# Kernel optimization log

Hardware: AMD Instinct MI355X
Metric: run time of the kernel (lower is better)

## Reference

```python
import jax, jax.numpy as jnp
import numpy as np

N, M, NTYPES, C, AXIS = 4096, 128, 2, 64, 16
TYPE_IDX = (0, 2048, 4096)        # atom-type partition along center axis
NTYPE_IDX = (0, 64, 128)          # neighbor-type partition along neighbor axis
RCUT = 6.0
BOX = 20.0
SR_MEAN = (0.1, 0.1)              # precomputed stats (get_stats)
SR_STD = (0.05, 0.05)
NORM = 20.0                       # avg neighbor count + 1


def setup_inputs() -> dict:
    key = jax.random.key(0)
    ks = jax.random.split(key, 16)
    coord_3N = jax.random.uniform(ks[0], (3, N), dtype=jnp.float32) * BOX
    box = jnp.full((3,), BOX, dtype=jnp.float32)
    # neighbors sorted by type: first 64 of type 0, last 64 of type 1
    nbr0 = jax.random.randint(ks[1], (N, M // 2), 0, TYPE_IDX[1])
    nbr1 = jax.random.randint(ks[2], (N, M // 2), TYPE_IDX[1], TYPE_IDX[2])
    nbrs_idx = jnp.concatenate([nbr0, nbr1], axis=1).astype(jnp.int32)
    # 4 per-(center,neighbor)-type embedding nets, widths 1->16->32->64, stacked
    eW0 = jax.random.normal(ks[3], (4, 1, 16), dtype=jnp.float32)
    eb0 = jax.random.normal(ks[4], (4, 16), dtype=jnp.float32) * 0.1
    eW1 = jax.random.normal(ks[5], (4, 16, 32), dtype=jnp.float32) / 4.0
    eb1 = jax.random.normal(ks[6], (4, 32), dtype=jnp.float32) * 0.1
    eW2 = jax.random.normal(ks[7], (4, 32, 64), dtype=jnp.float32) / (32.0 ** 0.5)
    eb2 = jax.random.normal(ks[8], (4, 64), dtype=jnp.float32) * 0.1
    Tbias = jnp.zeros((1, C), dtype=jnp.float32)
    # 2 per-type fitting nets, widths 1024->128->128->1, stacked
    fW0 = jax.random.normal(ks[9], (2, AXIS * C, 128), dtype=jnp.float32) / (AXIS * C) ** 0.5
    fb0 = jnp.zeros((2, 128), dtype=jnp.float32)
    fW1 = jax.random.normal(ks[10], (2, 128, 128), dtype=jnp.float32) / (128.0 ** 0.5)
    fb1 = jnp.zeros((2, 128), dtype=jnp.float32)
    fW2 = jax.random.normal(ks[11], (2, 128, 1), dtype=jnp.float32) / (128.0 ** 0.5)
    fb2 = jnp.zeros((2, 1), dtype=jnp.float32)
    Ebias = jnp.zeros((2,), dtype=jnp.float32)
    return {"coord_3N": coord_3N, "box": box, "nbrs_idx": nbrs_idx,
            "eW0": eW0, "eb0": eb0, "eW1": eW1, "eb1": eb1, "eW2": eW2, "eb2": eb2,
            "Tbias": Tbias, "fW0": fW0, "fb0": fb0, "fW1": fW1, "fb1": fb1,
            "fW2": fW2, "fb2": fb2, "Ebias": Ebias}


def reference(coord_3N, box, nbrs_idx, eW0, eb0, eW1, eb1, eW2, eb2,
              Tbias, fW0, fb0, fW1, fb1, fW2, fb2, Ebias):
    # --- neighbor gather + minimal-image relative coords (get_relative_coord) ---
    x_3NM = coord_3N[:, nbrs_idx] - coord_3N[:, :, None]            # [3,N,M]
    x_3NM = x_3NM - box[:, None, None] * jnp.round(x_3NM / box[:, None, None])
    r2 = (x_3NM ** 2).sum(0)
    mask = r2 > 1e-12
    rsafe = jnp.sqrt(jnp.where(mask, r2, 1.0))                      # safe for grads
    r_NM = jnp.where(mask, rsafe, 0.0)                              # [N,M]
    # --- smooth radial feature sr(r) = switch(r)/r ---
    sw = 0.5 * jnp.cos(jnp.pi * jnp.minimum(r_NM, RCUT) / RCUT) + 0.5
    sr_NM = jnp.where(mask & (r_NM < RCUT), sw / rsafe, 0.0)
    # --- per-center-type normalization (slice_t / concat_t over type_idx) ---
    srn_rows, srcn = [], []
    for i in range(NTYPES):
        blk = sr_NM[TYPE_IDX[i]:TYPE_IDX[i + 1]]
        srn_rows.append(blk / SR_STD[i])
        srcn.append((blk - SR_MEAN[i]) / SR_STD[i])
    sr_norm_NM = jnp.concatenate(srn_rows, 0)
    x_norm_3NM = x_3NM / jnp.where(mask, rsafe, 1.0)[None]
    R_3NM = 3 ** 0.5 * sr_norm_NM * x_norm_3NM
    R2diag_3NM = 9 ** 0.5 * sr_norm_NM * (x_norm_3NM ** 2 - 1.0 / 3.0)
    R2offd_3NM = 18 ** 0.5 * sr_norm_NM * (x_norm_3NM * jnp.stack([x_norm_3NM[1], x_norm_3NM[2], x_norm_3NM[0]]))
    R_XNM = jnp.concatenate([sr_norm_NM[None], R_3NM, R2diag_3NM, R2offd_3NM])  # [10,N,M]

    # --- per-(center,neighbor)-type embedding MLPs on scalar sr feature ---
    def embed(x, k):  # x: [n, m] -> [n, m, C]
        h = jnp.tanh(x[:, :, None] @ eW0[k] + eb0[k])
        h = jnp.tanh(h @ eW1[k] + eb1[k])
        return jnp.tanh(h @ eW2[k] + eb2[k])

    rows = []
    for i in range(NTYPES):
        cols = [embed(srcn[i][:, NTYPE_IDX[j]:NTYPE_IDX[j + 1]], i * NTYPES + j)
                for j in range(NTYPES)]
        rows.append(jnp.concatenate(cols, 1))
    embed_NMC = jnp.concatenate(rows, 0)                            # [N,M,C]

    # --- descriptor contraction ---
    T_NXC = jnp.einsum('xnm,nmc->nxc', R_XNM, embed_NMC) / NORM     # [N,10,C]
    T_NC = T_NXC[:, 0] + Tbias
    T_N3C = T_NXC[:, 1:4]
    T_N6C = T_NXC[:, 4:]
    G_NAC = T_NC[:, None] * T_NC[:, :AXIS, None] \
        + (T_N3C[:, :, None] * T_N3C[:, :, :AXIS, None]).sum(1)     # [N,AXIS,C]
    # use_2nd branch
    G1 = T_N3C[:, :, AXIS:2 * AXIS]                                 # [N,3,AXIS]
    G11 = jnp.concatenate([G1 ** 2,
                           2 ** 0.5 * G1 * jnp.stack([G1[:, 1], G1[:, 2], G1[:, 0]], axis=1)], axis=1)
    G2 = G11 + T_N6C[:, :, AXIS:2 * AXIS]                           # [N,6,AXIS]
    G_NAC = G_NAC + jnp.einsum('nxa,nxc->nac', G2, T_N6C)

    # --- per-type fitting nets ---
    Gflat = G_NAC.reshape(N, AXIS * C)
    energy = jnp.zeros((), dtype=Gflat.dtype)
    for t in range(NTYPES):
        g = Gflat[TYPE_IDX[t]:TYPE_IDX[t + 1]]
        h = jnp.tanh(g @ fW0[t] + fb0[t])
        h = jnp.tanh(h @ fW1[t] + fb1[t])
        f = h @ fW2[t] + fb2[t]
        energy = energy + (f + Ebias[t]).sum()
    return energy
```

## Files before the change

kernel.cpp:

```cpp
#include <hip/hip_runtime.h>
#include <hip/hip_fp16.h>

typedef _Float16 h16;
typedef h16 v2h __attribute__((ext_vector_type(2)));
typedef h16 v8h __attribute__((ext_vector_type(8)));
typedef float f4 __attribute__((ext_vector_type(4)));

#define NATOM 4096
#define HALF_N 2048
#define K2 2.885390081777927f
#define GSCL 0.015625f
#define W0SCL (64.0f * K2)

#define TBL_N 2048
#define W0MIN_ (-0.201f)
#define DW_ (1.2005f / 2047.0f)
#define RSCALE_ (2047.0f / 1.2005f)

__device__ __forceinline__ float rcp_fast(float x) {
#if __has_builtin(__builtin_amdgcn_rcpf)
  return __builtin_amdgcn_rcpf(x);
#else
  return 1.0f / x;
#endif
}

__device__ __forceinline__ float exp2_fast(float x) {
#if __has_builtin(__builtin_amdgcn_exp2f)
  return __builtin_amdgcn_exp2f(x);
#else
  return exp2f(x);
#endif
}

__device__ __forceinline__ float tanh_e2(float d) {
  float r = rcp_fast(1.0f + exp2_fast(d));
  return fmaf(-2.0f, r, 1.0f);
}

__device__ __forceinline__ v8h lds_v8h(const h16* base, int byte) {
  return *(const v8h*)((const char*)base + byte);
}

__global__ __launch_bounds__(256) void k_setup(
    const float* __restrict__ eW0, const float* __restrict__ eb0,
    const float* __restrict__ eW1, const float* __restrict__ eb1,
    const float* __restrict__ eW2, const float* __restrict__ eb2,
    const float* __restrict__ fW0, const float* __restrict__ coord,
    h16* __restrict__ tbl, h16* __restrict__ W0t, f4* __restrict__ coordP)
{
  const int bid = blockIdx.x, tid = threadIdx.x;
  if (bid < 512) {
    __shared__ float sW1[512];
    __shared__ float sW2[2048];
    __shared__ float sW0s[16], sb0s[16], sb1s[32], sb2s[64];
    const int net = bid >> 7;
    for (int i = tid; i < 512; i += 256) sW1[i] = eW1[net * 512 + i];
    for (int i = tid; i < 2048; i += 256) sW2[i] = eW2[net * 2048 + i];
    if (tid < 16) { sW0s[tid] = eW0[net * 16 + tid]; sb0s[tid] = eb0[net * 16 + tid]; }
    else if (tid >= 32 && tid < 64) sb1s[tid - 32] = eb1[net * 32 + tid - 32];
    else if (tid >= 64 && tid < 128) sb2s[tid - 64] = eb2[net * 64 + tid - 64];
    __syncthreads();

    const int u = (bid & 127) * 256 + tid;
    const int e = u >> 4, cq = u & 15;
    const float w = W0MIN_ + (float)e * DW_;
    const float s = 8.0f * w * rcp_fast(1.0f - fabsf(w));
    float h0[16];
#pragma unroll
    for (int i = 0; i < 16; ++i)
      h0[i] = tanh_e2(K2 * fmaf(s, sW0s[i], sb0s[i]));
    float h1[32];
#pragma unroll
    for (int j = 0; j < 32; ++j) {
      float a = sb1s[j];
#pragma unroll
      for (int i = 0; i < 16; ++i) a = fmaf(h0[i], sW1[i * 32 + j], a);
      h1[j] = tanh_e2(K2 * a);
    }
    f4 a4 = *(const f4*)&sb2s[cq * 4];
    for (int j = 0; j < 32; ++j) {
      f4 wv4 = *(const f4*)&sW2[j * 64 + cq * 4];
      a4 += h1[j] * wv4;
    }
    union { h16 e4[4]; unsigned long long q; } o;
#pragma unroll
    for (int q = 0; q < 4; ++q) o.e4[q] = (h16)tanh_e2(K2 * a4[q]);
    *(unsigned long long*)&tbl[((size_t)(net * TBL_N + e)) * 64 + cq * 4] = o.q;
  } else if (bid < 640) {
    int idx = (bid - 512) * 256 + tid;
    int t = idx >> 14, n = idx & 127, k8 = (idx >> 7) & 127;
    union { v8h v; h16 e[8]; } o;
#pragma unroll
    for (int i = 0; i < 8; ++i)
      o.e[i] = (h16)(W0SCL * fW0[(size_t)t * 131072 + (size_t)(k8 * 8 + i) * 128 + n]);
    *(v8h*)&W0t[((size_t)t * 128 + n) * 1024 + k8 * 8] = o.v;
  } else {
    int idx = (bid - 640) * 256 + tid;
    f4 c;
    c.x = coord[idx]; c.y = coord[NATOM + idx]; c.z = coord[2 * NATOM + idx];
    c.w = 0.0f;
    coordP[idx] = c;
  }
}

__global__ __launch_bounds__(256, 3) void k_embed(
    const f4* __restrict__ coordP, const float* __restrict__ box,
    const int* __restrict__ nbrs, const float* __restrict__ Tbias,
    const h16* __restrict__ tbl, h16* __restrict__ Gout)
{
  __shared__ h16   E32t[4][64][40] __attribute__((aligned(16)));
  __shared__ h16   Rls[4][10][136] __attribute__((aligned(16)));
  __shared__ float Tls[4][10][64];

  const int tid = threadIdx.x;
  const int wv = tid >> 6;
  const int lane = tid & 63;
  const int n = blockIdx.x * 4 + wv;
  const int ti = (n >= HALF_N) ? 1 : 0;
  const int c15 = lane & 15, g4 = lane >> 4;
  const int mloc = lane >> 1, hh = lane & 1;

  const int jnb0 = nbrs[(size_t)n * 128 + lane];
  const int jnb1 = nbrs[(size_t)n * 128 + 64 + lane];

  int uf0 = 0, uf1 = 0;
  {
    const float bx = box[0], by = box[1], bz = box[2];
    const float rbx = rcp_fast(bx), rby = rcp_fast(by), rbz = rcp_fast(bz);
    const f4 cme = coordP[n];
#pragma unroll
    for (int nb = 0; nb < 2; ++nb) {
      const int m = nb * 64 + lane;
      const f4 cj = coordP[nb ? jnb1 : jnb0];
      float dx = cj.x - cme.x;
      float dy = cj.y - cme.y;
      float dz = cj.z - cme.z;
      dx -= bx * rintf(dx * rbx);
      dy -= by * rintf(dy * rby);
      dz -= bz * rintf(dz * rbz);
      float r2 = dx * dx + dy * dy + dz * dz;
      bool mk = r2 > 1e-12f;
      float rs = sqrtf(mk ? r2 : 1.0f);
      float r  = mk ? rs : 0.0f;
      float sw = 0.5f * __cosf(0.52359878f * fminf(r, 6.0f)) + 0.5f;
      float invr = mk ? rcp_fast(rs) : 1.0f;
      float sr = (mk && r < 6.0f) ? sw * invr : 0.0f;
      float x0 = dx * invr, x1 = dy * invr, x2 = dz * invr;
      float srn = sr * 20.0f;
      float s   = (sr - 0.1f) * 20.0f;
      Rls[wv][0][m] = (h16)srn;
      Rls[wv][1][m] = (h16)(1.7320508f * srn * x0);
      Rls[wv][2][m] = (h16)(1.7320508f * srn * x1);
      Rls[wv][3][m] = (h16)(1.7320508f * srn * x2);
      Rls[wv][4][m] = (h16)(3.0f * srn * (x0 * x0 - 0.33333334f));
      Rls[wv][5][m] = (h16)(3.0f * srn * (x1 * x1 - 0.33333334f));
      Rls[wv][6][m] = (h16)(3.0f * srn * (x2 * x2 - 0.33333334f));
      Rls[wv][7][m] = (h16)(4.2426407f * srn * (x0 * x1));
      Rls[wv][8][m] = (h16)(4.2426407f * srn * (x1 * x2));
      Rls[wv][9][m] = (h16)(4.2426407f * srn * (x2 * x0));
      float wr = s * rcp_fast(8.0f + fabsf(s));
      float fidx = (wr - W0MIN_) * RSCALE_;
      fidx = fminf(fmaxf(fidx, 0.0f), 2045.99f);
      float i0f = floorf(fidx);
      h16 frh = (h16)(fidx - i0f);
      int uf = ((int)i0f << 16) |
               (int)__builtin_bit_cast(unsigned short, frh);
      if (nb == 0) uf0 = uf; else uf1 = uf;
    }
  }

  union U8 { v8h v; v2h p[4]; h16 e[8]; };
  const int rrow = (c15 < 10) ? c15 : 9;
  const v8h vzero = {};
  f4 tac[4];
#pragma unroll
  for (int nt = 0; nt < 4; ++nt) tac[nt] = (f4){0.f, 0.f, 0.f, 0.f};

  auto issue = [&](int ks, U8* buf) -> float {
    unsigned uu = (unsigned)__builtin_amdgcn_ds_bpermute(
        (((ks & 1) * 32) + mloc) * 4, (ks < 2) ? uf0 : uf1);
    int i0 = (int)(uu >> 16);
    float fr = (float)__builtin_bit_cast(h16, (unsigned short)(uu & 0xffffu));
    const int net = ti * 2 + (ks >> 1);
    const h16* rp = tbl + ((size_t)net * TBL_N + i0) * 64 + hh * 8;
#pragma unroll
    for (int q = 0; q < 4; ++q) {
      buf[q].v     = *(const v8h*)(rp + q * 16);
      buf[4 + q].v = *(const v8h*)(rp + 64 + q * 16);
    }
    return fr;
  };

  auto proc = [&](int ks, U8* buf, float fr) {
    v2h fr2; fr2.x = (h16)fr; fr2.y = (h16)fr;
#pragma unroll
    for (int q = 0; q < 4; ++q) {
#pragma unroll
      for (int p = 0; p < 4; ++p) {
        v2h d = buf[4 + q].p[p] - buf[q].p[p];
        v2h e2 = buf[q].p[p] + fr2 * d;
        const int ch = q * 16 + hh * 8 + p * 2;
        E32t[wv][ch][mloc]     = e2.x;
        E32t[wv][ch + 1][mloc] = e2.y;
      }
    }
    v8h ra = *(const v8h*)&Rls[wv][rrow][ks * 32 + g4 * 8];
    if (c15 >= 10) ra = vzero;
#pragma unroll
    for (int nt = 0; nt < 4; ++nt) {
      v8h bf = *(const v8h*)&E32t[wv][nt * 16 + c15][g4 * 8];
      tac[nt] = __builtin_amdgcn_mfma_f32_16x16x32_f16(ra, bf, tac[nt], 0, 0, 0);
    }
  };

  U8 bA[8], bB[8];
  float frA = issue(0, bA);
  float frB = issue(1, bB);
  proc(0, bA, frA);
  frA = issue(2, bA);
  proc(1, bB, frB);
  frB = issue(3, bB);
  proc(2, bA, frA);
  proc(3, bB, frB);

#pragma unroll
  for (int nt = 0; nt < 4; ++nt)
#pragma unroll
    for (int r = 0; r < 4; ++r) {
      int x = g4 * 4 + r;
      if (x < 10) Tls[wv][x][nt * 16 + c15] = tac[nt][r] * 0.05f;
    }

  {
    const int c = lane;
    const float tnc  = Tls[wv][0][c] + Tbias[c];
    const float t3c0 = Tls[wv][1][c], t3c1 = Tls[wv][2][c], t3c2 = Tls[wv][3][c];
    const float t6c0 = Tls[wv][4][c], t6c1 = Tls[wv][5][c], t6c2 = Tls[wv][6][c];
    const float t6c3 = Tls[wv][7][c], t6c4 = Tls[wv][8][c], t6c5 = Tls[wv][9][c];
    h16* gp = Gout + (size_t)n * 1024;
#pragma unroll
    for (int a = 0; a < 16; ++a) {
      float g = tnc * (Tls[wv][0][a] + Tbias[a]);
      g += t3c0 * Tls[wv][1][a] + t3c1 * Tls[wv][2][a] + t3c2 * Tls[wv][3][a];
      const float g1x = Tls[wv][1][16 + a], g1y = Tls[wv][2][16 + a], g1z = Tls[wv][3][16 + a];
      g += (g1x * g1x + Tls[wv][4][16 + a]) * t6c0;
      g += (g1y * g1y + Tls[wv][5][16 + a]) * t6c1;
      g += (g1z * g1z + Tls[wv][6][16 + a]) * t6c2;
      g += (1.4142135f * g1x * g1y + Tls[wv][7][16 + a]) * t6c3;
      g += (1.4142135f * g1y * g1z + Tls[wv][8][16 + a]) * t6c4;
      g += (1.4142135f * g1z * g1x + Tls[wv][9][16 + a]) * t6c5;
      gp[a * 64 + c] = (h16)(g * GSCL);
    }
  }
}

__global__ __launch_bounds__(256, 2) void k_fit0(
    const h16* __restrict__ G16, const h16* __restrict__ W0t,
    float* __restrict__ P)
{
  __shared__ h16 As[32][64]  __attribute__((aligned(16)));
  __shared__ h16 Bts[128][64] __attribute__((aligned(16)));
  const int tid = threadIdx.x;
  const int tile = blockIdx.x >> 2;
  const int ks = blockIdx.x & 3;
  const int abase = tile * 32;
  const int kbase = ks * 256;
  const int t = (abase >= HALF_N) ? 1 : 0;
  const int lane = tid & 63, w = tid >> 6;
  const int c15 = lane & 15, g4 = lane >> 4;
  const int mrow = (w & 1) * 16, nh = (w >> 1) * 64;

  f4 acc[4];
#pragma unroll
  for (int nt = 0; nt < 4; ++nt) acc[nt] = (f4){0.f, 0.f, 0.f, 0.f};

  for (int kc = 0; kc < 4; ++kc) {
    const int kb = kbase + kc * 64;
    __syncthreads();
    {
      int r = tid >> 3, c8 = tid & 7;
      v8h v = *(const v8h*)&G16[(size_t)(abase + r) * 1024 + kb + c8 * 8];
      int byte = r * 128 + ((c8 * 16) ^ ((r & 7) << 4));
      *(v8h*)((char*)&As[0][0] + byte) = v;
    }
#pragma unroll
    for (int u = 0; u < 4; ++u) {
      int idx = u * 256 + tid;
      int nr = idx >> 3, c8 = idx & 7;
      v8h v = *(const v8h*)&W0t[((size_t)t * 128 + nr) * 1024 + kb + c8 * 8];
      int byte = nr * 128 + ((c8 * 16) ^ ((nr & 7) << 4));
      *(v8h*)((char*)&Bts[0][0] + byte) = v;
    }
    __syncthreads();
#pragma unroll
    for (int ksub = 0; ksub < 2; ++ksub) {
      const int ar = mrow + c15;
      const int koff = (ksub * 32 + g4 * 8) * 2;
      v8h a = lds_v8h(&As[0][0], ar * 128 + (koff ^ ((ar & 7) << 4)));
#pragma unroll
      for (int nt = 0; nt < 4; ++nt) {
        const int br = nh + nt * 16 + c15;
        v8h b = lds_v8h(&Bts[0][0], br * 128 + (koff ^ ((br & 7) << 4)));
        acc[nt] = __builtin_amdgcn_mfma_f32_16x16x32_f16(a, b, acc[nt], 0, 0, 0);
      }
    }
  }

  float* Pk = P + (size_t)ks * 4096 * 128;
#pragma unroll
  for (int nt = 0; nt < 4; ++nt)
#pragma unroll
    for (int r = 0; r < 4; ++r)
      Pk[(size_t)(abase + mrow + g4 * 4 + r) * 128 + nh + nt * 16 + c15] = acc[nt][r];
}

__global__ __launch_bounds__(256, 4) void k_fit1(
    const float* __restrict__ P,
    const float* __restrict__ fb0, const float* __restrict__ fW1,
    const float* __restrict__ fb1, const float* __restrict__ fW2,
    const float* __restrict__ fb2, const float* __restrict__ Ebias,
    float* __restrict__ BP)
{
  __shared__ float ht[128][12];
  __shared__ float Ws1[32][128];
  __shared__ float red[8][33];
  const int tid = threadIdx.x;
  const int abase = blockIdx.x * 8;
  const int t = (abase >= HALF_N) ? 1 : 0;

  {
    const int a = tid >> 5, j0 = (tid & 31) * 4;
    f4 s = K2 * (*(const f4*)&fb0[t * 128 + j0]);
#pragma unroll
    for (int ks = 0; ks < 4; ++ks)
      s += *(const f4*)&P[((size_t)ks * 4096 + abase + a) * 128 + j0];
    ht[j0 + 0][a] = tanh_e2(s.x);
    ht[j0 + 1][a] = tanh_e2(s.y);
    ht[j0 + 2][a] = tanh_e2(s.z);
    ht[j0 + 3][a] = tanh_e2(s.w);
  }

  const int ab = tid & 7, jb = tid >> 3;
  const int j0g = jb * 4;
  f4 acc = K2 * (*(const f4*)&fb1[t * 128 + j0g]);
  for (int kc = 0; kc < 4; ++kc) {
    __syncthreads();
#pragma unroll
    for (int u = 0; u < 2; ++u) {
      int idx = (u * 256 + tid) * 8;
      int kk = idx >> 7, j = idx & 127;
      *(f4*)&Ws1[kk][j] =
          K2 * (*(const f4*)&fW1[(size_t)t * 16384 + (size_t)(kc * 32 + kk) * 128 + j]);
      *(f4*)&Ws1[kk][j + 4] =
          K2 * (*(const f4*)&fW1[(size_t)t * 16384 + (size_t)(kc * 32 + kk) * 128 + j + 4]);
    }
    __syncthreads();
    for (int kk = 0; kk < 32; ++kk) {
      float av = ht[kc * 32 + kk][ab];
      f4 w = *(const f4*)&Ws1[kk][j0g];
      acc += av * w;
    }
  }

  float f = tanh_e2(acc.x) * fW2[t * 128 + j0g + 0]
          + tanh_e2(acc.y) * fW2[t * 128 + j0g + 1]
          + tanh_e2(acc.z) * fW2[t * 128 + j0g + 2]
          + tanh_e2(acc.w) * fW2[t * 128 + j0g + 3];
  red[ab][jb] = f;
  __syncthreads();
  if (tid < 64) {
    const int a = tid & 7, j4 = tid >> 3;
    float v = red[a][j4 * 4] + red[a][j4 * 4 + 1]
            + red[a][j4 * 4 + 2] + red[a][j4 * 4 + 3];
    v += __shfl_xor(v, 32);
    v += __shfl_xor(v, 16);
    v += __shfl_xor(v, 8);
    v += __shfl_xor(v, 4);
    v += __shfl_xor(v, 2);
    v += __shfl_xor(v, 1);
    if (tid == 0) BP[blockIdx.x] = v + 8.0f * (fb2[t] + Ebias[t]);
  }
}

__global__ __launch_bounds__(64) void k_reduce(const float* __restrict__ BP,
                                               float* __restrict__ out)
{
  int tid = threadIdx.x;
  float s = 0.0f;
#pragma unroll
  for (int u = 0; u < 8; ++u) s += BP[tid + 64 * u];
  s += __shfl_xor(s, 32);
  s += __shfl_xor(s, 16);
  s += __shfl_xor(s, 8);
  s += __shfl_xor(s, 4);
  s += __shfl_xor(s, 2);
  s += __shfl_xor(s, 1);
  if (tid == 0) out[0] = s;
}

extern "C" void kernel_launch(void* const* d_in, const int* in_sizes, int n_in,
                              void* d_out, int out_size, void* d_ws, size_t ws_size,
                              hipStream_t stream) {
  const float* coord = (const float*)d_in[0];
  const float* box   = (const float*)d_in[1];
  const int*   nbrs  = (const int*)d_in[2];
  const float* eW0   = (const float*)d_in[3];
  const float* eb0   = (const float*)d_in[4];
  const float* eW1   = (const float*)d_in[5];
  const float* eb1   = (const float*)d_in[6];
  const float* eW2   = (const float*)d_in[7];
  const float* eb2   = (const float*)d_in[8];
  const float* Tbias = (const float*)d_in[9];
  const float* fW0   = (const float*)d_in[10];
  const float* fb0   = (const float*)d_in[11];
  const float* fW1   = (const float*)d_in[12];
  const float* fb1   = (const float*)d_in[13];
  const float* fW2   = (const float*)d_in[14];
  const float* fb2   = (const float*)d_in[15];
  const float* Ebias = (const float*)d_in[16];

  h16*   G16 = (h16*)d_ws;
  float* P   = (float*)((char*)d_ws + (size_t)8 * 1024 * 1024);
  h16*   W0t = (h16*)((char*)d_ws + (size_t)16 * 1024 * 1024);
  float* BP  = (float*)((char*)d_ws + (size_t)17 * 1024 * 1024);
  h16*   tbl = (h16*)((char*)d_ws + (size_t)18 * 1024 * 1024);
  f4*    cP  = (f4*)((char*)d_ws + (size_t)19 * 1024 * 1024);

  k_setup<<<656, 256, 0, stream>>>(eW0, eb0, eW1, eb1, eW2, eb2, fW0, coord,
                                   tbl, W0t, cP);
  k_embed<<<1024, 256, 0, stream>>>(cP, box, nbrs, Tbias, tbl, G16);
  k_fit0<<<512, 256, 0, stream>>>(G16, W0t, P);
  k_fit1<<<512, 256, 0, stream>>>(P, fb0, fW1, fb1, fW2, fb2, Ebias, BP);
  k_reduce<<<1, 64, 0, stream>>>(BP, (float*)d_out);
}
```

Baseline: 45.87 us.

## Fuse fitting-net layers into one MFMA kernel with double-buffered K loop

Merges the split-K first fitting layer and the scalar second layer into a single kernel. Each block computes a 32-atom tile over the full K=1024 with double-buffered LDS staging, applies tanh, then runs the 128x128 second layer with fp16 MFMA against a pre-transposed W1 and reduces in place. This removes the fp32 partial-sum round trip through global memory and one kernel launch. In exchange the fused kernel launches only 128 blocks, so many CUs sit idle, and the second layer now uses fp16 instead of fp32. The embed kernel's launch bound also changes from 3 to 2 blocks per CU.

New measurement: 44.84 us. 1.02x faster.

```diff
diff --git a/kernel.cpp b/kernel.cpp
--- a/kernel.cpp
+++ b/kernel.cpp
@@ -46,8 +46,10 @@
     const float* __restrict__ eW0, const float* __restrict__ eb0,
     const float* __restrict__ eW1, const float* __restrict__ eb1,
     const float* __restrict__ eW2, const float* __restrict__ eb2,
-    const float* __restrict__ fW0, const float* __restrict__ coord,
-    h16* __restrict__ tbl, h16* __restrict__ W0t, f4* __restrict__ coordP)
+    const float* __restrict__ fW0, const float* __restrict__ fW1,
+    const float* __restrict__ coord,
+    h16* __restrict__ tbl, h16* __restrict__ W0t, h16* __restrict__ W1t,
+    f4* __restrict__ coordP)
 {
   const int bid = blockIdx.x, tid = threadIdx.x;
   if (bid < 512) {
@@ -95,16 +97,25 @@
     for (int i = 0; i < 8; ++i)
       o.e[i] = (h16)(W0SCL * fW0[(size_t)t * 131072 + (size_t)(k8 * 8 + i) * 128 + n]);
     *(v8h*)&W0t[((size_t)t * 128 + n) * 1024 + k8 * 8] = o.v;
-  } else {
+  } else if (bid < 656) {
     int idx = (bid - 640) * 256 + tid;
     f4 c;
     c.x = coord[idx]; c.y = coord[NATOM + idx]; c.z = coord[2 * NATOM + idx];
     c.w = 0.0f;
     coordP[idx] = c;
-  }
-}
-
-__global__ __launch_bounds__(256, 3) void k_embed(
+  } else {
+    int idx = (bid - 656) * 256 + tid;
+    int t = idx >> 11, rem = idx & 2047;
+    int n = rem >> 4, k8 = rem & 15;
+    union { v8h v; h16 e[8]; } o;
+#pragma unroll
+    for (int i = 0; i < 8; ++i)
+      o.e[i] = (h16)(K2 * fW1[(size_t)t * 16384 + (size_t)(k8 * 8 + i) * 128 + n]);
+    *(v8h*)&W1t[((size_t)t * 128 + n) * 128 + k8 * 8] = o.v;
+  }
+}
+
+__global__ __launch_bounds__(256, 2) void k_embed(
     const f4* __restrict__ coordP, const float* __restrict__ box,
     const int* __restrict__ nbrs, const float* __restrict__ Tbias,
     const h16* __restrict__ tbl, h16* __restrict__ Gout)
@@ -255,131 +266,134 @@
   }
 }
 
-__global__ __launch_bounds__(256, 2) void k_fit0(
+__global__ __launch_bounds__(256) void k_fit(
     const h16* __restrict__ G16, const h16* __restrict__ W0t,
-    float* __restrict__ P)
+    const h16* __restrict__ W1t,
+    const float* __restrict__ fb0, const float* __restrict__ fb1,
+    const float* __restrict__ fW2, const float* __restrict__ fb2,
+    const float* __restrict__ Ebias, float* __restrict__ BP)
 {
-  __shared__ h16 As[32][64]  __attribute__((aligned(16)));
-  __shared__ h16 Bts[128][64] __attribute__((aligned(16)));
+  __shared__ h16 As[2][32][64]  __attribute__((aligned(16)));
+  __shared__ h16 Bs[2][128][64] __attribute__((aligned(16)));
+  __shared__ h16 ht[32][128]    __attribute__((aligned(16)));
+  __shared__ h16 W1s[128][128]  __attribute__((aligned(16)));
+  __shared__ float red[32][33];
+
   const int tid = threadIdx.x;
-  const int tile = blockIdx.x >> 2;
-  const int ks = blockIdx.x & 3;
-  const int abase = tile * 32;
-  const int kbase = ks * 256;
+  const int abase = blockIdx.x * 32;
   const int t = (abase >= HALF_N) ? 1 : 0;
   const int lane = tid & 63, w = tid >> 6;
   const int c15 = lane & 15, g4 = lane >> 4;
-  const int mrow = (w & 1) * 16, nh = (w >> 1) * 64;
+  const int rt = w & 1, ng = w >> 1;
+
+  float fb0v[4], b1v[4], w2v[4];
+#pragma unroll
+  for (int nt = 0; nt < 4; ++nt) {
+    const int nn = ng * 64 + nt * 16 + c15;
+    fb0v[nt] = K2 * fb0[t * 128 + nn];
+    b1v[nt]  = K2 * fb1[t * 128 + nn];
+    w2v[nt]  = fW2[t * 128 + nn];
+  }
+
+#pragma unroll
+  for (int u = 0; u < 8; ++u) {
+    int idx = u * 256 + tid;
+    int nrow = idx >> 4, c8 = idx & 15;
+    v8h v = *(const v8h*)&W1t[((size_t)t * 128 + nrow) * 128 + c8 * 8];
+    int byte = nrow * 256 + ((c8 * 16) ^ ((nrow & 7) << 4));
+    *(v8h*)((char*)&W1s[0][0] + byte) = v;
+  }
 
   f4 acc[4];
 #pragma unroll
   for (int nt = 0; nt < 4; ++nt) acc[nt] = (f4){0.f, 0.f, 0.f, 0.f};
 
-  for (int kc = 0; kc < 4; ++kc) {
-    const int kb = kbase + kc * 64;
-    __syncthreads();
+  auto stageK = [&](int kc, int p) {
     {
       int r = tid >> 3, c8 = tid & 7;
-      v8h v = *(const v8h*)&G16[(size_t)(abase + r) * 1024 + kb + c8 * 8];
+      v8h v = *(const v8h*)&G16[(size_t)(abase + r) * 1024 + kc * 64 + c8 * 8];
       int byte = r * 128 + ((c8 * 16) ^ ((r & 7) << 4));
-      *(v8h*)((char*)&As[0][0] + byte) = v;
+      *(v8h*)((char*)&As[p][0][0] + byte) = v;
     }
 #pragma unroll
     for (int u = 0; u < 4; ++u) {
       int idx = u * 256 + tid;
-      int nr = idx >> 3, c8 = idx & 7;
-      v8h v = *(const v8h*)&W0t[((size_t)t * 128 + nr) * 1024 + kb + c8 * 8];
-      int byte = nr * 128 + ((c8 * 16) ^ ((nr & 7) << 4));
-      *(v8h*)((char*)&Bts[0][0] + byte) = v;
-    }
-    __syncthreads();
+      int nrow = idx >> 3, c8 = idx & 7;
+      v8h v = *(const v8h*)&W0t[((size_t)t * 128 + nrow) * 1024 + kc * 64 + c8 * 8];
+      int byte = nrow * 128 + ((c8 * 16) ^ ((nrow & 7) << 4));
+      *(v8h*)((char*)&Bs[p][0][0] + byte) = v;
+    }
+  };
+
+  stageK(0, 0);
+  __syncthreads();
+  for (int kc = 0; kc < 16; ++kc) {
+    const int p = kc & 1;
+    if (kc < 15) stageK(kc + 1, p ^ 1);
 #pragma unroll
     for (int ksub = 0; ksub < 2; ++ksub) {
-      const int ar = mrow + c15;
+      const int ar = rt * 16 + c15;
       const int koff = (ksub * 32 + g4 * 8) * 2;
-      v8h a = lds_v8h(&As[0][0], ar * 128 + (koff ^ ((ar & 7) << 4)));
+      v8h a = lds_v8h(&As[p][0][0], ar * 128 + (koff ^ ((ar & 7) << 4)));
 #pragma unroll
       for (int nt = 0; nt < 4; ++nt) {
-        const int br = nh + nt * 16 + c15;
-        v8h b = lds_v8h(&Bts[0][0], br * 128 + (koff ^ ((br & 7) << 4)));
+        const int br = ng * 64 + nt * 16 + c15;
+        v8h b = lds_v8h(&Bs[p][0][0], br * 128 + (koff ^ ((br & 7) << 4)));
         acc[nt] = __builtin_amdgcn_mfma_f32_16x16x32_f16(a, b, acc[nt], 0, 0, 0);
       }
     }
-  }
-
-  float* Pk = P + (size_t)ks * 4096 * 128;
+    __syncthreads();
+  }
+
 #pragma unroll
   for (int nt = 0; nt < 4; ++nt)
 #pragma unroll
-    for (int r = 0; r < 4; ++r)
-      Pk[(size_t)(abase + mrow + g4 * 4 + r) * 128 + nh + nt * 16 + c15] = acc[nt][r];
-}
-
-__global__ __launch_bounds__(256, 4) void k_fit1(
-    const float* __restrict__ P,
-    const float* __restrict__ fb0, const float* __restrict__ fW1,
-    const float* __restrict__ fb1, const float* __restrict__ fW2,
-    const float* __restrict__ fb2, const float* __restrict__ Ebias,
-    float* __restrict__ BP)
-{
-  __shared__ float ht[128][12];
-  __shared__ float Ws1[32][128];
-  __shared__ float red[8][33];
-  const int tid = threadIdx.x;
-  const int abase = blockIdx.x * 8;
-  const int t = (abase >= HALF_N) ? 1 : 0;
-
-  {
-    const int a = tid >> 5, j0 = (tid & 31) * 4;
-    f4 s = K2 * (*(const f4*)&fb0[t * 128 + j0]);
-#pragma unroll
-    for (int ks = 0; ks < 4; ++ks)
-      s += *(const f4*)&P[((size_t)ks * 4096 + abase + a) * 128 + j0];
-    ht[j0 + 0][a] = tanh_e2(s.x);
-    ht[j0 + 1][a] = tanh_e2(s.y);
-    ht[j0 + 2][a] = tanh_e2(s.z);
-    ht[j0 + 3][a] = tanh_e2(s.w);
-  }
-
-  const int ab = tid & 7, jb = tid >> 3;
-  const int j0g = jb * 4;
-  f4 acc = K2 * (*(const f4*)&fb1[t * 128 + j0g]);
-  for (int kc = 0; kc < 4; ++kc) {
-    __syncthreads();
-#pragma unroll
-    for (int u = 0; u < 2; ++u) {
-      int idx = (u * 256 + tid) * 8;
-      int kk = idx >> 7, j = idx & 127;
-      *(f4*)&Ws1[kk][j] =
-          K2 * (*(const f4*)&fW1[(size_t)t * 16384 + (size_t)(kc * 32 + kk) * 128 + j]);
-      *(f4*)&Ws1[kk][j + 4] =
-          K2 * (*(const f4*)&fW1[(size_t)t * 16384 + (size_t)(kc * 32 + kk) * 128 + j + 4]);
-    }
-    __syncthreads();
-    for (int kk = 0; kk < 32; ++kk) {
-      float av = ht[kc * 32 + kk][ab];
-      f4 w = *(const f4*)&Ws1[kk][j0g];
-      acc += av * w;
-    }
-  }
-
-  float f = tanh_e2(acc.x) * fW2[t * 128 + j0g + 0]
-          + tanh_e2(acc.y) * fW2[t * 128 + j0g + 1]
-          + tanh_e2(acc.z) * fW2[t * 128 + j0g + 2]
-          + tanh_e2(acc.w) * fW2[t * 128 + j0g + 3];
-  red[ab][jb] = f;
+    for (int r = 0; r < 4; ++r) {
+      int a = rt * 16 + g4 * 4 + r;
+      int k = ng * 64 + nt * 16 + c15;
+      h16 hv = (h16)tanh_e2(acc[nt][r] + fb0v[nt]);
+      int byte = a * 256 + ((k * 2) ^ ((a & 7) << 4));
+      *((h16*)((char*)&ht[0][0] + byte)) = hv;
+    }
+  __syncthreads();
+
+  f4 acc2[4];
+#pragma unroll
+  for (int nt = 0; nt < 4; ++nt) acc2[nt] = (f4){0.f, 0.f, 0.f, 0.f};
+#pragma unroll
+  for (int ks2 = 0; ks2 < 4; ++ks2) {
+    const int ar = rt * 16 + c15;
+    const int koff = (ks2 * 32 + g4 * 8) * 2;
+    v8h a = lds_v8h(&ht[0][0], ar * 256 + (koff ^ ((ar & 7) << 4)));
+#pragma unroll
+    for (int nt = 0; nt < 4; ++nt) {
+      const int br = ng * 64 + nt * 16 + c15;
+      v8h b = lds_v8h(&W1s[0][0], br * 256 + (koff ^ ((br & 7) << 4)));
+      acc2[nt] = __builtin_amdgcn_mfma_f32_16x16x32_f16(a, b, acc2[nt], 0, 0, 0);
+    }
+  }
+
+#pragma unroll
+  for (int r = 0; r < 4; ++r) {
+    float v = 0.0f;
+#pragma unroll
+    for (int nt = 0; nt < 4; ++nt)
+      v += tanh_e2(acc2[nt][r] + b1v[nt]) * w2v[nt];
+    red[rt * 16 + g4 * 4 + r][ng * 16 + c15] = v;
+  }
   __syncthreads();
   if (tid < 64) {
-    const int a = tid & 7, j4 = tid >> 3;
-    float v = red[a][j4 * 4] + red[a][j4 * 4 + 1]
-            + red[a][j4 * 4 + 2] + red[a][j4 * 4 + 3];
-    v += __shfl_xor(v, 32);
-    v += __shfl_xor(v, 16);
-    v += __shfl_xor(v, 8);
-    v += __shfl_xor(v, 4);
-    v += __shfl_xor(v, 2);
-    v += __shfl_xor(v, 1);
-    if (tid == 0) BP[blockIdx.x] = v + 8.0f * (fb2[t] + Ebias[t]);
+    const int a = tid & 31, half = tid >> 5;
+    float s = 0.0f;
+#pragma unroll
+    for (int c = 0; c < 16; ++c) s += red[a][half * 16 + c];
+    s += __shfl_xor(s, 32);
+    s += __shfl_xor(s, 16);
+    s += __shfl_xor(s, 8);
+    s += __shfl_xor(s, 4);
+    s += __shfl_xor(s, 2);
+    s += __shfl_xor(s, 1);
+    if (tid == 0) BP[blockIdx.x] = s + 32.0f * (fb2[t] + Ebias[t]);
   }
 }
 
@@ -387,9 +401,7 @@
                                                float* __restrict__ out)
 {
   int tid = threadIdx.x;
-  float s = 0.0f;
-#pragma unroll
-  for (int u = 0; u < 8; ++u) s += BP[tid + 64 * u];
+  float s = BP[tid] + BP[tid + 64];
   s += __shfl_xor(s, 32);
   s += __shfl_xor(s, 16);
   s += __shfl_xor(s, 8);
@@ -420,17 +432,17 @@
   const float* fb2   = (const float*)d_in[15];
   const float* Ebias = (const float*)d_in[16];
 
-  h16*   G16 = (h16*)d_ws;
-  float* P   = (float*)((char*)d_ws + (size_t)8 * 1024 * 1024);
-  h16*   W0t = (h16*)((char*)d_ws + (size_t)16 * 1024 * 1024);
-  float* BP  = (float*)((char*)d_ws + (size_t)17 * 1024 * 1024);
-  h16*   tbl = (h16*)((char*)d_ws + (size_t)18 * 1024 * 1024);
-  f4*    cP  = (f4*)((char*)d_ws + (size_t)19 * 1024 * 1024);
-
-  k_setup<<<656, 256, 0, stream>>>(eW0, eb0, eW1, eb1, eW2, eb2, fW0, coord,
-                                   tbl, W0t, cP);
+  char* ws = (char*)d_ws;
+  h16*   G16 = (h16*)ws;
+  h16*   W0t = (h16*)(ws + (size_t)8  * 1024 * 1024);
+  h16*   W1t = (h16*)(ws + (size_t)9  * 1024 * 1024);
+  h16*   tbl = (h16*)(ws + (size_t)10 * 1024 * 1024);
+  f4*    cP  = (f4*)(ws + (size_t)11 * 1024 * 1024);
+  float* BP  = (float*)(ws + (size_t)12 * 1024 * 1024);
+
+  k_setup<<<672, 256, 0, stream>>>(eW0, eb0, eW1, eb1, eW2, eb2, fW0, fW1,
+                                   coord, tbl, W0t, W1t, cP);
   k_embed<<<1024, 256, 0, stream>>>(cP, box, nbrs, Tbias, tbl, G16);
-  k_fit0<<<512, 256, 0, stream>>>(G16, W0t, P);
-  k_fit1<<<512, 256, 0, stream>>>(P, fb0, fW1, fb1, fW2, fb2, Ebias, BP);
+  k_fit<<<128, 256, 0, stream>>>(G16, W0t, W1t, fb0, fb1, fW2, fb2, Ebias, BP);
   k_reduce<<<1, 64, 0, stream>>>(BP, (float*)d_out);
 }
```
